# Kernel optimization log

Hardware: AMD Instinct MI355X
Metric: run time of the kernel (lower is better)

The kernel has to match this reference:

```python
import jax, jax.numpy as jnp
import numpy as np

LEN = 16384
TAU = 20.0
DT = 1.0


def setup_inputs() -> dict:
    key = jax.random.key(0)
    k1, k2 = jax.random.split(key)
    inp = jax.random.normal(k1, (1024, 1, LEN), dtype=jnp.float32)
    tgt = jax.random.normal(k2, (1024, 1, LEN), dtype=jnp.float32)
    return {"input": inp, "target": tgt}


def _exp_causal_filter(x, decay):
    # x: [B, 1, L]. Causal exponential filter:
    #   y[t] = sum_{m=0}^{t} x[t-m] * decay**m  ==  y[t] = decay*y[t-1] + x[t]
    # This is exactly conv1d(pad(x, (L-1, 0)), kernel=[exp(-t/tau) for t in L-1..0]).
    def step(carry, xt):
        y = decay * carry + xt
        return y, y

    x_t = jnp.moveaxis(x, -1, 0)  # [L, B, 1]
    y0 = jnp.zeros(x.shape[:-1], x.dtype)  # [B, 1]
    _, ys = jax.lax.scan(step, y0, x_t)  # [L, B, 1]
    return jnp.moveaxis(ys, 0, -1)  # [B, 1, L]


def reference(input, target):
    decay = jnp.exp(jnp.asarray(-DT * 0.0 - 1.0 / TAU, input.dtype))  # exp(-1/tau)
    diff = input - target
    filtered = _exp_causal_filter(diff, decay)
    return jnp.sqrt((1.0 / TAU) * jnp.sum(filtered * filtered) * DT)
```

## Files before the change

kernel.cpp:

```cpp
#include <hip/hip_runtime.h>
#include <math.h>

#define LEN       16384
#define NTHREADS  1024
#define SEG       16
#define NWAVES    16

#define DECAY_F 0.951229424500714f
#define D16_F   0.449328964117222f
#define G16_F   7.5886329f

__device__ __forceinline__ int swz(int a) { return a ^ ((a >> 5) & 31); }

__global__ __launch_bounds__(NTHREADS) void vr_main(
    const float* __restrict__ in, const float* __restrict__ tgt,
    float* __restrict__ partial)
{
    __shared__ float smem[LEN];
    __shared__ float wa[NWAVES], wb[NWAVES], red[NWAVES];

    const int row = blockIdx.x;
    const int tid = threadIdx.x;
    const long long rb = (long long)row * LEN;
    const float4* __restrict__ in4 = (const float4*)(in  + rb);
    const float4* __restrict__ tg4 = (const float4*)(tgt + rb);

    #pragma unroll
    for (int p = 0; p < LEN / 4 / NTHREADS; ++p) {
        const int idx4 = tid + p * NTHREADS;
        const float4 a = in4[idx4];
        const float4 b = tg4[idx4];
        const int base = idx4 * 4;
        smem[swz(base + 0)] = a.x - b.x;
        smem[swz(base + 1)] = a.y - b.y;
        smem[swz(base + 2)] = a.z - b.z;
        smem[swz(base + 3)] = a.w - b.w;
    }
    __syncthreads();

    float s = 0.f, A = 0.f, Bc = 0.f, w = 1.f;
    const int base = tid * SEG;
    #pragma unroll
    for (int i = 0; i < SEG; ++i) {
        const float x = smem[swz(base + i)];
        s = __builtin_fmaf(DECAY_F, s, x);
        w *= DECAY_F;
        A  = __builtin_fmaf(s, s, A);
        Bc = __builtin_fmaf(w, s, Bc);
    }

    float a = D16_F;
    float b = s;
    const int lane = tid & 63;
    #pragma unroll
    for (int j = 1; j < 64; j <<= 1) {
        const float au = __shfl_up(a, j);
        const float bu = __shfl_up(b, j);
        if (lane >= j) {
            b = __builtin_fmaf(a, bu, b);
            a *= au;
        }
    }
    const int wid = tid >> 6;
    if (lane == 63) { wa[wid] = a; wb[wid] = b; }
    __syncthreads();

    float C = 0.f;
    for (int k = 0; k < wid; ++k) C = __builtin_fmaf(wa[k], C, wb[k]);
    float aex = __shfl_up(a, 1);
    float bex = __shfl_up(b, 1);
    if (lane == 0) { aex = 1.f; bex = 0.f; }
    const float c = __builtin_fmaf(aex, C, bex);

    float part = A + 2.f * c * Bc + (c * c) * G16_F;

    #pragma unroll
    for (int j = 32; j > 0; j >>= 1) part += __shfl_down(part, j);
    if (lane == 0) red[wid] = part;
    __syncthreads();
    if (tid == 0) {
        float t = 0.f;
        #pragma unroll
        for (int k = 0; k < NWAVES; ++k) t += red[k];
        partial[row] = t;
    }
}

__global__ __launch_bounds__(1024) void vr_final(
    const float* __restrict__ partial, int n, float* __restrict__ out)
{
    __shared__ float red[16];
    const int tid = threadIdx.x;
    float v = 0.f;
    for (int k = tid; k < n; k += 1024) v += partial[k];
    #pragma unroll
    for (int j = 32; j > 0; j >>= 1) v += __shfl_down(v, j);
    const int lane = tid & 63, wid = tid >> 6;
    if (lane == 0) red[wid] = v;
    __syncthreads();
    if (tid == 0) {
        float t = 0.f;
        #pragma unroll
        for (int k = 0; k < 16; ++k) t += red[k];
        out[0] = sqrtf(t * 0.05f);
    }
}

extern "C" void kernel_launch(void* const* d_in, const int* in_sizes, int n_in,
                              void* d_out, int out_size, void* d_ws, size_t ws_size,
                              hipStream_t stream) {
    const float* in  = (const float*)d_in[0];
    const float* tgt = (const float*)d_in[1];
    float* out = (float*)d_out;
    float* ws  = (float*)d_ws;
    const int rows = in_sizes[0] / LEN;

    vr_main<<<dim3(rows), dim3(NTHREADS), 0, stream>>>(in, tgt, ws);
    vr_final<<<dim3(1), dim3(1024), 0, stream>>>(ws, rows, out);
}
```

Baseline: 28.21 us.

## Fuse final reduction via last-block counter and load segments directly into registers

Each thread now loads its own 16 contiguous elements straight from global memory into registers instead of staging the row through swizzled shared memory. This removes 64KB of LDS per block and one barrier, which can raise occupancy. The separate final-reduction kernel is replaced by an atomic counter, so the last block to finish sums the partials. This adds a memset launch, and the final reduction only covers up to 1024 rows. The per-thread loads are strided by 64 bytes across lanes, so they coalesce less well.

```diff
diff --git a/kernel.cpp b/kernel.cpp
--- a/kernel.cpp
+++ b/kernel.cpp
@@ -10,44 +10,31 @@
 #define D16_F   0.449328964117222f
 #define G16_F   7.5886329f
 
-__device__ __forceinline__ int swz(int a) { return a ^ ((a >> 5) & 31); }
+#define STEP(xv) { s = __builtin_fmaf(DECAY_F, s, (xv)); w *= DECAY_F; \
+                   A = __builtin_fmaf(s, s, A); Bc = __builtin_fmaf(w, s, Bc); }
 
-__global__ __launch_bounds__(NTHREADS) void vr_main(
+__global__ __launch_bounds__(NTHREADS) void vr_fused(
     const float* __restrict__ in, const float* __restrict__ tgt,
-    float* __restrict__ partial)
+    float* __restrict__ partial, unsigned int* __restrict__ counter,
+    float* __restrict__ out, int nrows)
 {
-    __shared__ float smem[LEN];
     __shared__ float wa[NWAVES], wb[NWAVES], red[NWAVES];
+    __shared__ int lastdone;
 
     const int row = blockIdx.x;
     const int tid = threadIdx.x;
-    const long long rb = (long long)row * LEN;
+    const long long rb = (long long)row * LEN + (long long)tid * SEG;
     const float4* __restrict__ in4 = (const float4*)(in  + rb);
     const float4* __restrict__ tg4 = (const float4*)(tgt + rb);
 
-    #pragma unroll
-    for (int p = 0; p < LEN / 4 / NTHREADS; ++p) {
-        const int idx4 = tid + p * NTHREADS;
-        const float4 a = in4[idx4];
-        const float4 b = tg4[idx4];
-        const int base = idx4 * 4;
-        smem[swz(base + 0)] = a.x - b.x;
-        smem[swz(base + 1)] = a.y - b.y;
-        smem[swz(base + 2)] = a.z - b.z;
-        smem[swz(base + 3)] = a.w - b.w;
-    }
-    __syncthreads();
+    const float4 a0 = in4[0], a1 = in4[1], a2 = in4[2], a3 = in4[3];
+    const float4 b0 = tg4[0], b1 = tg4[1], b2 = tg4[2], b3 = tg4[3];
 
     float s = 0.f, A = 0.f, Bc = 0.f, w = 1.f;
-    const int base = tid * SEG;
-    #pragma unroll
-    for (int i = 0; i < SEG; ++i) {
-        const float x = smem[swz(base + i)];
-        s = __builtin_fmaf(DECAY_F, s, x);
-        w *= DECAY_F;
-        A  = __builtin_fmaf(s, s, A);
-        Bc = __builtin_fmaf(w, s, Bc);
-    }
+    STEP(a0.x - b0.x) STEP(a0.y - b0.y) STEP(a0.z - b0.z) STEP(a0.w - b0.w)
+    STEP(a1.x - b1.x) STEP(a1.y - b1.y) STEP(a1.z - b1.z) STEP(a1.w - b1.w)
+    STEP(a2.x - b2.x) STEP(a2.y - b2.y) STEP(a2.z - b2.z) STEP(a2.w - b2.w)
+    STEP(a3.x - b3.x) STEP(a3.y - b3.y) STEP(a3.z - b3.z) STEP(a3.w - b3.w)
 
     float a = D16_F;
     float b = s;
@@ -82,27 +69,29 @@
         float t = 0.f;
         #pragma unroll
         for (int k = 0; k < NWAVES; ++k) t += red[k];
-        partial[row] = t;
+        __hip_atomic_store(&partial[row], t, __ATOMIC_RELEASE,
+                           __HIP_MEMORY_SCOPE_AGENT);
+        const unsigned int old = __hip_atomic_fetch_add(
+            counter, 1u, __ATOMIC_ACQ_REL, __HIP_MEMORY_SCOPE_AGENT);
+        lastdone = (old == (unsigned int)(nrows - 1)) ? 1 : 0;
     }
-}
+    __syncthreads();
 
-__global__ __launch_bounds__(1024) void vr_final(
-    const float* __restrict__ partial, int n, float* __restrict__ out)
-{
-    __shared__ float red[16];
-    const int tid = threadIdx.x;
-    float v = 0.f;
-    for (int k = tid; k < n; k += 1024) v += partial[k];
-    #pragma unroll
-    for (int j = 32; j > 0; j >>= 1) v += __shfl_down(v, j);
-    const int lane = tid & 63, wid = tid >> 6;
-    if (lane == 0) red[wid] = v;
-    __syncthreads();
-    if (tid == 0) {
-        float t = 0.f;
+    if (lastdone) {
+        float v = (tid < nrows)
+            ? __hip_atomic_load(&partial[tid], __ATOMIC_RELAXED,
+                                __HIP_MEMORY_SCOPE_AGENT)
+            : 0.f;
         #pragma unroll
-        for (int k = 0; k < 16; ++k) t += red[k];
-        out[0] = sqrtf(t * 0.05f);
+        for (int j = 32; j > 0; j >>= 1) v += __shfl_down(v, j);
+        if (lane == 0) red[wid] = v;
+        __syncthreads();
+        if (tid == 0) {
+            float t = 0.f;
+            #pragma unroll
+            for (int k = 0; k < NWAVES; ++k) t += red[k];
+            out[0] = sqrtf(t * 0.05f);
+        }
     }
 }
 
@@ -112,9 +101,11 @@
     const float* in  = (const float*)d_in[0];
     const float* tgt = (const float*)d_in[1];
     float* out = (float*)d_out;
-    float* ws  = (float*)d_ws;
+    float* partial = (float*)d_ws;
     const int rows = in_sizes[0] / LEN;
+    unsigned int* counter = (unsigned int*)(partial + rows);
 
-    vr_main<<<dim3(rows), dim3(NTHREADS), 0, stream>>>(in, tgt, ws);
-    vr_final<<<dim3(1), dim3(1024), 0, stream>>>(ws, rows, out);
+    hipMemsetAsync(counter, 0, sizeof(unsigned int), stream);
+    vr_fused<<<dim3(rows), dim3(NTHREADS), 0, stream>>>(
+        in, tgt, partial, counter, out, rows);
 }
```

Measured after the change: 75.33 us. 167% more time.
